# Performance work log

Measured on AMD Instinct MI355X. Metric: run time of the kernel, lower is better.

Reference implementation:

```python
import jax, jax.numpy as jnp
import numpy as np

N = 500_000      # num nodes
E = 8_000_000    # num edges (before self-loops)
F_IN, H, C = 16, 8, 2


def setup_inputs() -> dict:
    key = jax.random.key(0)
    k = jax.random.split(key, 6)
    x = jax.random.normal(k[0], (N, F_IN), dtype=jnp.float32)
    edge_index = jax.random.randint(k[1], (2, E), 0, N, dtype=jnp.int32)
    # Glorot-style init like PyG GCNConv
    W1 = jax.random.normal(k[2], (F_IN, H), dtype=jnp.float32) * (1.0 / np.sqrt(F_IN))
    b1 = jnp.zeros((H,), dtype=jnp.float32)
    W2 = jax.random.normal(k[3], (H, C), dtype=jnp.float32) * (1.0 / np.sqrt(H))
    b2 = jnp.zeros((C,), dtype=jnp.float32)
    return {"x": x, "W1": W1, "b1": b1, "W2": W2, "b2": b2, "edge_index": edge_index}


def reference(x, W1, b1, W2, b2, edge_index):
    # GCNConv: out = D^{-1/2} (A + I) D^{-1/2} X W + b   (PyG semantics)
    row, col = edge_index[0], edge_index[1]           # messages flow row -> col
    loop = jnp.arange(N, dtype=row.dtype)
    row = jnp.concatenate([row, loop])                # add self-loops
    col = jnp.concatenate([col, loop])
    deg = jax.ops.segment_sum(jnp.ones_like(col, dtype=x.dtype), col, num_segments=N)
    dinv = jnp.where(deg > 0, jax.lax.rsqrt(deg), jnp.zeros_like(deg))
    norm = dinv[row] * dinv[col]                      # [E+N]

    def propagate(h):  # h: [N, d] -> normalized scatter-add aggregation
        msg = h[row] * norm[:, None]                  # gather + scale, [E+N, d]
        return jax.ops.segment_sum(msg, col, num_segments=N)

    h = jax.nn.relu(propagate(x @ W1) + b1)           # [N, 8]
    out = propagate(h @ W2) + b2                      # [N, 2]
    return jax.nn.log_softmax(out, axis=1)
```

## Files before the change

### kernel.cpp

```cpp
#include <hip/hip_runtime.h>

#define TPB 256
#define NBLK_EDGE 512
#define CHUNKE 16384
#define BIN_SHIFT 9
#define BIN_SIZE 512
#define MAXK 1024
#define ROW_BITS 19
#define ROW_MASK ((1u << ROW_BITS) - 1)
#define Q_SHIFT 17
#define NKEY 2048
#define CAP 12288
#define G1_TPB 512

typedef _Float16 half8  __attribute__((ext_vector_type(8)));
typedef _Float16 half2v __attribute__((ext_vector_type(2)));

__device__ __forceinline__ int wave_scan_incl(int v, int lane) {
#pragma unroll
    for (int d = 1; d < 64; d <<= 1) {
        int u = __shfl_up(v, d, 64);
        if (lane >= d) v += u;
    }
    return v;
}

__device__ __forceinline__ int block_excl_scan_1024(int v, int tid, int* wsum) {
    int lane = tid & 63, wv = tid >> 6;
    int incl = wave_scan_incl(v, lane);
    if (lane == 63) wsum[wv] = incl;
    __syncthreads();
    if (tid < 16) {
        int w = wsum[tid];
#pragma unroll
        for (int d = 1; d < 16; d <<= 1) {
            int u = __shfl_up(w, d, 16);
            if (tid >= d) w += u;
        }
        wsum[tid] = w;
    }
    __syncthreads();
    return incl - v + (wv ? wsum[wv - 1] : 0);
}

__global__ void __launch_bounds__(1024) k_hist(
        const int* __restrict__ col, int E, int chunk,
        int* __restrict__ cntB, int* __restrict__ cntT) {
    __shared__ int lh[MAXK];
    int blk = blockIdx.x, tid = threadIdx.x;
    lh[tid] = 0;
    __syncthreads();
    int s = blk * chunk, e_ = min(s + chunk, E);
    for (int e = s + tid; e < e_; e += 1024)
        atomicAdd(&lh[col[e] >> BIN_SHIFT], 1);
    __syncthreads();
    int v = lh[tid];
    cntB[(size_t)blk * MAXK + tid] = v;
    cntT[(size_t)tid * NBLK_EDGE + blk] = v;
}

__global__ void k_colscan(int* __restrict__ cntT, int* __restrict__ ghist) {
    __shared__ int part[256];
    int b = blockIdx.x, tid = threadIdx.x;
    size_t base = (size_t)b * NBLK_EDGE;
    int t2 = tid * 2;
    int c0 = cntT[base + t2], c1 = cntT[base + t2 + 1];
    int sum = c0 + c1;
    part[tid] = sum;
    __syncthreads();
    for (int off = 1; off < 256; off <<= 1) {
        int v = (tid >= off) ? part[tid - off] : 0;
        __syncthreads();
        part[tid] += v;
        __syncthreads();
    }
    int excl = part[tid] - sum;
    cntT[base + t2]     = excl;
    cntT[base + t2 + 1] = excl + c0;
    if (tid == 255) ghist[b] = part[255];
}

__global__ void __launch_bounds__(1024) k_scan(
        const int* __restrict__ ghist, int K, int* __restrict__ binBase,
        int* __restrict__ scratchCur) {
    __shared__ int wsum[16];
    int tid = threadIdx.x;
    if (tid == 0) *scratchCur = 0;
    int val = (tid < K) ? ghist[tid] : 0;
    int excl = block_excl_scan_1024(val, tid, wsum);
    binBase[tid] = excl;
    if (tid == K - 1) binBase[K] = excl + val;
}

__global__ void __launch_bounds__(1024) k_reorder(
        const int* __restrict__ row, const int* __restrict__ col,
        int E, int chunk,
        const int* __restrict__ binBase, const int* __restrict__ cntB,
        const int* __restrict__ cntT, unsigned* __restrict__ packed) {
    __shared__ unsigned sorted[CHUNKE];
    __shared__ unsigned short sbin[CHUNKE];
    __shared__ int lcur[MAXK], lbase[MAXK], gbase[MAXK];
    __shared__ int wsum[16];
    int blk = blockIdx.x, tid = threadIdx.x;
    int s = blk * chunk, e_ = min(s + chunk, E), len = e_ - s;
    size_t bb = (size_t)blk * MAXK;
    int c0 = cntB[bb + tid];
    int excl = block_excl_scan_1024(c0, tid, wsum);
    lbase[tid] = excl;
    lcur[tid] = excl;
    gbase[tid] = binBase[tid] + cntT[(size_t)tid * NBLK_EDGE + blk];
    __syncthreads();
    for (int i = tid; i < len; i += blockDim.x) {
        int cc = col[s + i];
        int b = cc >> BIN_SHIFT;
        int slot = atomicAdd(&lcur[b], 1);
        sorted[slot] = ((unsigned)(cc & (BIN_SIZE - 1)) << ROW_BITS) | (unsigned)row[s + i];
        sbin[slot] = (unsigned short)b;
    }
    __syncthreads();
    for (int i = tid; i < len; i += blockDim.x) {
        int b = sbin[i];
        packed[gbase[b] + (i - lbase[b])] = sorted[i];
    }
}

__global__ void __launch_bounds__(1024) k_binsort(
        unsigned* __restrict__ packed, const int* __restrict__ binBase,
        unsigned* __restrict__ scratch, int* __restrict__ scratchCur,
        const float* __restrict__ x, const float* __restrict__ W1,
        half8* __restrict__ g0, int* __restrict__ keyptr, int N, int E, int K) {
    __shared__ unsigned buf2[CAP];
    __shared__ int cnt[NKEY], cur[NKEY];
    __shared__ float w1s[128];
    __shared__ int wsum[16];
    __shared__ int sbShared;
    int tid = threadIdx.x;
    int bin = blockIdx.x;
    int s = binBase[bin], t = binBase[bin + 1];
    int len = t - s;
    bool fast = (len <= CAP);
    cnt[tid] = 0;
    cnt[tid + 1024] = 0;
    if (tid < 128) w1s[tid] = W1[tid];
    if (!fast && tid == 0) sbShared = atomicAdd(scratchCur, len);
    __syncthreads();
    for (int i = tid; i < len; i += 1024) {
        unsigned v = packed[s + i];
        int k = (int)((v >> ROW_BITS) << 2) | (int)((v & ROW_MASK) >> Q_SHIFT);
        atomicAdd(&cnt[k], 1);
    }
    __syncthreads();
    int t2 = tid * 2;
    int c0 = cnt[t2], c1 = cnt[t2 + 1];
    int excl = block_excl_scan_1024(c0 + c1, tid, wsum);
    cur[t2] = excl;
    cur[t2 + 1] = excl + c0;
    int base = bin << BIN_SHIFT;
    if (base + (t2 >> 2) < N) keyptr[((size_t)bin << 11) + t2] = s + excl;
    if (base + ((t2 + 1) >> 2) < N) keyptr[((size_t)bin << 11) + t2 + 1] = s + excl + c0;
    float di = 0.0f;
    int node = base + tid;
    if (tid < BIN_SIZE && node < N) {
        int deg = cnt[4 * tid] + cnt[4 * tid + 1] + cnt[4 * tid + 2] + cnt[4 * tid + 3];
        di = rsqrtf((float)(deg + 1));
    }
    if (bin == K - 1 && tid == 0) keyptr[(size_t)4 * N] = E;
    __syncthreads();
    if (fast) {
        for (int i = tid; i < len; i += 1024) {
            unsigned v = packed[s + i];
            int k = (int)((v >> ROW_BITS) << 2) | (int)((v & ROW_MASK) >> Q_SHIFT);
            int slot = atomicAdd(&cur[k], 1);
            buf2[slot] = v;
        }
        __syncthreads();
        for (int i = tid; i < len; i += 1024) packed[s + i] = buf2[i];
    } else {
        unsigned* stg = scratch + sbShared;
        for (int i = tid; i < len; i += 1024) stg[i] = packed[s + i];
        __threadfence();
        __syncthreads();
        for (int i = tid; i < len; i += 1024) {
            unsigned v = stg[i];
            int k = (int)((v >> ROW_BITS) << 2) | (int)((v & ROW_MASK) >> Q_SHIFT);
            int slot = atomicAdd(&cur[k], 1);
            packed[s + slot] = v;
        }
    }
    if (tid < BIN_SIZE && node < N) {
        const float4* xv = (const float4*)(x + (size_t)node * 16);
        float h[8];
#pragma unroll
        for (int j = 0; j < 8; ++j) h[j] = 0.0f;
#pragma unroll
        for (int kk = 0; kk < 4; ++kk) {
            float4 a = xv[kk];
            int kb = kk * 4;
#pragma unroll
            for (int j = 0; j < 8; ++j)
                h[j] += a.x * w1s[kb * 8 + j] + a.y * w1s[(kb + 1) * 8 + j]
                      + a.z * w1s[(kb + 2) * 8 + j] + a.w * w1s[(kb + 3) * 8 + j];
        }
        half8 g;
#pragma unroll
        for (int j = 0; j < 8; ++j) g[j] = (_Float16)(di * h[j]);
        g0[node] = g;
    }
}

__global__ void __launch_bounds__(G1_TPB, 8) k_gather1(
        const unsigned* __restrict__ packed, const int* __restrict__ keyptr,
        const half8* __restrict__ g0, const float* __restrict__ b1,
        const float* __restrict__ W2, half2v* __restrict__ g1, int N) {
    int i = blockIdx.x * G1_TPB + threadIdx.x;
    bool act = (i < N);
    int kp0 = 0, kp1 = 0, kp2 = 0, kp3 = 0, kp4 = 0;
    if (act) {
        int4 k4 = ((const int4*)keyptr)[i];
        kp0 = k4.x; kp1 = k4.y; kp2 = k4.z; kp3 = k4.w;
        kp4 = keyptr[4 * i + 4];
    }
    float acc[8];
#pragma unroll
    for (int j = 0; j < 8; ++j) acc[j] = 0.0f;
#pragma unroll
    for (int q = 0; q < 4; ++q) {
        int e = (q == 0) ? kp0 : (q == 1) ? kp1 : (q == 2) ? kp2 : kp3;
        int t = (q == 0) ? kp1 : (q == 1) ? kp2 : (q == 2) ? kp3 : kp4;
        if (act) {
            for (; e + 4 <= t; e += 4) {
                unsigned p0 = packed[e], p1 = packed[e + 1],
                         p2 = packed[e + 2], p3 = packed[e + 3];
                half8 v0 = g0[p0 & ROW_MASK];
                half8 v1 = g0[p1 & ROW_MASK];
                half8 v2 = g0[p2 & ROW_MASK];
                half8 v3 = g0[p3 & ROW_MASK];
#pragma unroll
                for (int j = 0; j < 8; ++j)
                    acc[j] += (float)v0[j] + (float)v1[j] + (float)v2[j] + (float)v3[j];
            }
            for (; e < t; ++e) {
                half8 v = g0[packed[e] & ROW_MASK];
#pragma unroll
                for (int j = 0; j < 8; ++j) acc[j] += (float)v[j];
            }
        }
        __syncthreads();
    }
    if (act) {
        half8 self = g0[i];
        float di = rsqrtf((float)(kp4 - kp0 + 1));
        float o0 = 0.0f, o1 = 0.0f;
#pragma unroll
        for (int j = 0; j < 8; ++j) {
            float hj = fmaxf(di * (acc[j] + (float)self[j]) + b1[j], 0.0f);
            o0 += hj * W2[j * 2 + 0];
            o1 += hj * W2[j * 2 + 1];
        }
        half2v g;
        g.x = (_Float16)(di * o0);
        g.y = (_Float16)(di * o1);
        g1[i] = g;
    }
}

__global__ void __launch_bounds__(TPB) k_gather2(
        const unsigned* __restrict__ packed, const int* __restrict__ keyptr,
        const half2v* __restrict__ g1, const float* __restrict__ b2,
        float* __restrict__ out, int N) {
    int i = blockIdx.x * blockDim.x + threadIdx.x;
    if (i >= N) return;
    int s = keyptr[4 * i], t = keyptr[4 * i + 4];
    half2v sg = g1[i];
    float a0 = (float)sg.x, a1 = (float)sg.y;
    int e = s;
    for (; e + 4 <= t; e += 4) {
        unsigned p0 = packed[e], p1 = packed[e + 1], p2 = packed[e + 2], p3 = packed[e + 3];
        half2v v0 = g1[p0 & ROW_MASK];
        half2v v1 = g1[p1 & ROW_MASK];
        half2v v2 = g1[p2 & ROW_MASK];
        half2v v3 = g1[p3 & ROW_MASK];
        a0 += (float)v0.x + (float)v1.x + (float)v2.x + (float)v3.x;
        a1 += (float)v0.y + (float)v1.y + (float)v2.y + (float)v3.y;
    }
    for (; e < t; ++e) {
        half2v v = g1[packed[e] & ROW_MASK];
        a0 += (float)v.x;
        a1 += (float)v.y;
    }
    float di = rsqrtf((float)(t - s + 1));
    float o0 = di * a0 + b2[0];
    float o1 = di * a1 + b2[1];
    float m = fmaxf(o0, o1);
    float lse = m + logf(expf(o0 - m) + expf(o1 - m));
    ((float2*)out)[i] = make_float2(o0 - lse, o1 - lse);
}

extern "C" void kernel_launch(void* const* d_in, const int* in_sizes, int n_in,
                              void* d_out, int out_size, void* d_ws, size_t ws_size,
                              hipStream_t stream) {
    const float* x  = (const float*)d_in[0];
    const float* W1 = (const float*)d_in[1];
    const float* b1 = (const float*)d_in[2];
    const float* W2 = (const float*)d_in[3];
    const float* b2 = (const float*)d_in[4];
    const int*   ei = (const int*)d_in[5];

    const int N = in_sizes[0] / 16;
    const int E = in_sizes[5] / 2;
    const int* row = ei;
    const int* col = ei + E;
    const int K = (N + BIN_SIZE - 1) >> BIN_SHIFT;

    float* ws   = (float*)d_ws;
    half8* g0   = (half8*)ws;
    half2v* g1  = (half2v*)(ws + (size_t)4 * N);
    unsigned* scratch = (unsigned*)(ws + (size_t)5 * N);
    int* keyptr = (int*)(ws + (size_t)13 * N);
    int*   meta = (int*)(ws + (size_t)17 * N + 8);
    int* ghist      = meta;
    int* binBase    = meta + MAXK;
    int* scratchCur = meta + 2 * MAXK + 16;
    unsigned* packed = (unsigned*)(meta + 3 * MAXK);
    int* cntB = (int*)(packed + E);
    int* cntT = cntB + (size_t)MAXK * NBLK_EDGE;

    float* out = (float*)d_out;

    const int gN = (N + TPB - 1) / TPB;
    const int g1N = (N + G1_TPB - 1) / G1_TPB;
    const int chunk = (E + NBLK_EDGE - 1) / NBLK_EDGE;

    k_hist   <<<NBLK_EDGE, 1024, 0, stream>>>(col, E, chunk, cntB, cntT);
    k_colscan<<<K, 256, 0, stream>>>(cntT, ghist);
    k_scan   <<<1, MAXK, 0, stream>>>(ghist, K, binBase, scratchCur);
    k_reorder<<<NBLK_EDGE, 1024, 0, stream>>>(row, col, E, chunk,
                                              binBase, cntB, cntT, packed);
    k_binsort<<<K, 1024, 0, stream>>>(packed, binBase, scratch, scratchCur,
                                      x, W1, g0, keyptr, N, E, K);
    k_gather1<<<g1N, G1_TPB, 0, stream>>>(packed, keyptr, g0, b1, W2, g1, N);
    k_gather2<<<gN, TPB, 0, stream>>>(packed, keyptr, g1, b2, out, N);
}
```

Baseline: 340.4 us.

## Pace gather1 quarter-phases with a grid-wide spin barrier for cache locality

Result: no change. 342.7 us (+0.7%).

```diff
diff --git a/kernel.cpp b/kernel.cpp
--- a/kernel.cpp
+++ b/kernel.cpp
@@ -12,6 +12,7 @@
 #define NKEY 2048
 #define CAP 12288
 #define G1_TPB 512
+#define SPIN_CAP 20000
 
 typedef _Float16 half8  __attribute__((ext_vector_type(8)));
 typedef _Float16 half2v __attribute__((ext_vector_type(2)));
@@ -82,10 +83,10 @@
 
 __global__ void __launch_bounds__(1024) k_scan(
         const int* __restrict__ ghist, int K, int* __restrict__ binBase,
-        int* __restrict__ scratchCur) {
+        int* __restrict__ scratchCur, int* __restrict__ barCtr) {
     __shared__ int wsum[16];
     int tid = threadIdx.x;
-    if (tid == 0) *scratchCur = 0;
+    if (tid == 0) { *scratchCur = 0; *barCtr = 0; }
     int val = (tid < K) ? ghist[tid] : 0;
     int excl = block_excl_scan_1024(val, tid, wsum);
     binBase[tid] = excl;
@@ -211,8 +212,10 @@
 __global__ void __launch_bounds__(G1_TPB, 8) k_gather1(
         const unsigned* __restrict__ packed, const int* __restrict__ keyptr,
         const half8* __restrict__ g0, const float* __restrict__ b1,
-        const float* __restrict__ W2, half2v* __restrict__ g1, int N) {
-    int i = blockIdx.x * G1_TPB + threadIdx.x;
+        const float* __restrict__ W2, half2v* __restrict__ g1,
+        int* __restrict__ barCtr, int nblk, int N) {
+    int tid = threadIdx.x;
+    int i = blockIdx.x * G1_TPB + tid;
     bool act = (i < N);
     int kp0 = 0, kp1 = 0, kp2 = 0, kp3 = 0, kp4 = 0;
     if (act) {
@@ -245,7 +248,23 @@
                 for (int j = 0; j < 8; ++j) acc[j] += (float)v[j];
             }
         }
-        __syncthreads();
+        if (q < 3 && nblk > 0) {
+            __syncthreads();
+            if (tid == 0) {
+                __hip_atomic_fetch_add(barCtr, 1, __ATOMIC_RELAXED,
+                                       __HIP_MEMORY_SCOPE_AGENT);
+                int target = nblk * (q + 1);
+                for (int sp = 0; sp < SPIN_CAP; ++sp) {
+                    if (__hip_atomic_load(barCtr, __ATOMIC_RELAXED,
+                                          __HIP_MEMORY_SCOPE_AGENT) >= target)
+                        break;
+                    __builtin_amdgcn_s_sleep(2);
+                }
+            }
+            __syncthreads();
+        } else {
+            __syncthreads();
+        }
     }
     if (act) {
         half8 self = g0[i];
@@ -321,6 +340,7 @@
     int* ghist      = meta;
     int* binBase    = meta + MAXK;
     int* scratchCur = meta + 2 * MAXK + 16;
+    int* barCtr     = meta + 2 * MAXK + 64;
     unsigned* packed = (unsigned*)(meta + 3 * MAXK);
     int* cntB = (int*)(packed + E);
     int* cntT = cntB + (size_t)MAXK * NBLK_EDGE;
@@ -331,13 +351,27 @@
     const int g1N = (N + G1_TPB - 1) / G1_TPB;
     const int chunk = (E + NBLK_EDGE - 1) / NBLK_EDGE;
 
+    static int coop_capacity = -1;
+    if (coop_capacity < 0) {
+        int nb = 0;
+        if (hipOccupancyMaxActiveBlocksPerMultiprocessor(&nb, k_gather1,
+                                                         G1_TPB, 0) != hipSuccess)
+            nb = 0;
+        hipDeviceProp_t prop;
+        int ncu = 0;
+        if (hipGetDeviceProperties(&prop, 0) == hipSuccess) ncu = prop.multiProcessorCount;
+        coop_capacity = nb * ncu;
+    }
+    const int paceN = (coop_capacity >= g1N) ? g1N : 0;
+
     k_hist   <<<NBLK_EDGE, 1024, 0, stream>>>(col, E, chunk, cntB, cntT);
     k_colscan<<<K, 256, 0, stream>>>(cntT, ghist);
-    k_scan   <<<1, MAXK, 0, stream>>>(ghist, K, binBase, scratchCur);
+    k_scan   <<<1, MAXK, 0, stream>>>(ghist, K, binBase, scratchCur, barCtr);
     k_reorder<<<NBLK_EDGE, 1024, 0, stream>>>(row, col, E, chunk,
                                               binBase, cntB, cntT, packed);
     k_binsort<<<K, 1024, 0, stream>>>(packed, binBase, scratch, scratchCur,
                                       x, W1, g0, keyptr, N, E, K);
-    k_gather1<<<g1N, G1_TPB, 0, stream>>>(packed, keyptr, g0, b1, W2, g1, N);
+    k_gather1<<<g1N, G1_TPB, 0, stream>>>(packed, keyptr, g0, b1, W2, g1,
+                                          barCtr, paceN, N);
     k_gather2<<<gN, TPB, 0, stream>>>(packed, keyptr, g1, b2, out, N);
 }
```
